# Kernel optimization log

Hardware: AMD Instinct MI355X
Metric: run time of the kernel (lower is better)

Reference implementation:

```python
import jax, jax.numpy as jnp
import numpy as np

B, L, N, C = 8, 33600, 128, 80
ALPHA, BETA, TOPK, EPS = 1.0, 6.0, 13, 1e-9


def setup_inputs() -> dict:
    key = jax.random.key(0)
    ks = jax.random.split(key, 7)
    pred_scores = jax.random.uniform(ks[0], (B, L, C), jnp.float32)  # post-sigmoid scores
    pc = jax.random.uniform(ks[1], (B, L, 2), jnp.float32) * 1024.0
    pwh = jax.random.uniform(ks[2], (B, L, 2), jnp.float32) * 128.0 + 8.0
    pred_boxes = jnp.concatenate([pc - pwh / 2, pc + pwh / 2], axis=-1)  # xyxy
    gc = jax.random.uniform(ks[3], (B, N, 2), jnp.float32) * 1024.0
    gwh = jax.random.uniform(ks[4], (B, N, 2), jnp.float32) * 256.0 + 16.0
    gt_boxes = jnp.concatenate([gc - gwh / 2, gc + gwh / 2], axis=-1)  # xyxy
    anchor_points = jax.random.uniform(ks[5], (1, L, 2), jnp.float32) * 1024.0
    gt_labels = jax.random.randint(ks[6], (B, N, 1), 0, C).astype(jnp.int64)
    # last quarter of GT slots are padding
    pad_gt_mask = (jnp.arange(N)[None, :, None] < 96).astype(jnp.float32)
    pad_gt_mask = jnp.broadcast_to(pad_gt_mask, (B, N, 1))
    return {"pred_scores": pred_scores, "pred_boxes": pred_boxes,
            "anchor_points": anchor_points, "gt_labels": gt_labels,
            "gt_boxes": gt_boxes, "pad_gt_mask": pad_gt_mask, "bg_index": C}


def _pairwise_iou(gt, pr):
    # gt: [B,N,4], pr: [B,L,4] xyxy -> iou [B,N,L]
    lt = jnp.maximum(gt[:, :, None, :2], pr[:, None, :, :2])
    rb = jnp.minimum(gt[:, :, None, 2:], pr[:, None, :, 2:])
    wh = jnp.clip(rb - lt, 0.0)
    inter = wh[..., 0] * wh[..., 1]
    area_g = ((gt[..., 2] - gt[..., 0]) * (gt[..., 3] - gt[..., 1]))[:, :, None]
    area_p = ((pr[..., 2] - pr[..., 0]) * (pr[..., 3] - pr[..., 1]))[:, None, :]
    iou = inter / (area_g + area_p - inter + EPS)
    iou = jnp.where(iou > 1.0 + EPS, 0.0, iou)
    return jnp.clip(jnp.nan_to_num(iou), 0.0, 1.0)


def reference(pred_scores, pred_boxes, anchor_points, gt_labels, gt_boxes, pad_gt_mask, bg_index):
    b, l, c = pred_scores.shape
    n = gt_boxes.shape[1]
    iou = _pairwise_iou(gt_boxes, pred_boxes)  # [B,N,L]

    # spatial containment of anchor points in horizontal gt boxes -> [B,N,L]
    pts = anchor_points[0]  # [L,2]
    spatial = ((pts[None, None, :, 0] >= gt_boxes[:, :, None, 0]) &
               (pts[None, None, :, 0] <= gt_boxes[:, :, None, 2]) &
               (pts[None, None, :, 1] >= gt_boxes[:, :, None, 1]) &
               (pts[None, None, :, 1] <= gt_boxes[:, :, None, 3]))

    # gather per-GT class scores: class_scores[b,n,l] = pred_scores[b,l,label[b,n]]
    lbl = jnp.clip(gt_labels[..., 0], 0, c - 1)  # [B,N]
    ps_t = jnp.transpose(pred_scores, (0, 2, 1))  # [B,C,L]
    class_scores = jnp.take_along_axis(ps_t, jnp.broadcast_to(lbl[:, :, None], (b, n, l)), axis=1)

    align = (class_scores ** ALPHA) * (iou ** BETA)  # [B,N,L]

    # top-k per GT over anchors
    k = min(TOPK, l)
    s = align * spatial.astype(align.dtype)
    _, topk_idx = jax.lax.top_k(s, k)  # [B,N,k]
    bidx = jnp.arange(b)[:, None, None]
    gidx = jnp.arange(n)[None, :, None]
    topk_mask = jnp.zeros((b, n, l), bool).at[bidx, gidx, topk_idx].set(True)
    topk_mask = topk_mask & (pad_gt_mask[..., 0] > 0)[:, :, None]

    positive = topk_mask.astype(align.dtype) * spatial.astype(align.dtype) * pad_gt_mask

    # conflict resolution: anchors matched to >1 GT keep only the best-IoU GT
    conflict = positive.sum(axis=1) > 1  # [B,L]
    best_gt = jnp.argmax(iou, axis=1)  # [B,L]
    best_mask = (jnp.arange(n)[None, :, None] == best_gt[:, None, :])  # [B,N,L]
    positive = jnp.where(conflict[:, None, :], positive * best_mask.astype(positive.dtype), positive)

    has_assign = positive.sum(axis=1) > 0  # [B,L]
    gt_idx = jnp.argmax(positive, axis=1)  # [B,L]
    assigned_labels = jnp.take_along_axis(gt_labels[..., 0], gt_idx, axis=1)  # [B,L]
    assigned_labels = jnp.where(has_assign, assigned_labels, bg_index)
    assigned_boxes = jnp.take_along_axis(gt_boxes, jnp.broadcast_to(gt_idx[:, :, None], (b, l, 4)), axis=1)

    masked_align = align * positive
    max_align = masked_align.max(axis=-1, keepdims=True)  # [B,N,1]
    max_iou = (iou * positive).max(axis=-1, keepdims=True)  # [B,N,1]
    norm_align = masked_align / (max_align + EPS) * max_iou
    norm_factor = norm_align.max(axis=1)  # [B,L]
    # scatter score at assigned class; bg labels (== C) one-hot to all-zero row
    assigned_scores = jax.nn.one_hot(assigned_labels, c, dtype=pred_scores.dtype)
    assigned_scores = assigned_scores * (norm_factor * has_assign.astype(norm_factor.dtype))[:, :, None]
    return assigned_labels, assigned_boxes, assigned_scores
```

## Files before the change

kernel.cpp:

```cpp
#include <hip/hip_runtime.h>
#include <cstdint>
#include <cstddef>

#define B_DIM 8
#define L_DIM 33600
#define N_DIM 128
#define C_DIM 80
#define K_TOP 13
#define EPS_F 1e-9f
#define CAP 4096

__device__ __forceinline__ float iou_pair(float g0, float g1, float g2, float g3,
                                          float p0, float p1, float p2, float p3) {
    float ltx = fmaxf(g0, p0), lty = fmaxf(g1, p1);
    float rbx = fminf(g2, p2), rby = fminf(g3, p3);
    float wx = fmaxf(__fsub_rn(rbx, ltx), 0.0f);
    float wy = fmaxf(__fsub_rn(rby, lty), 0.0f);
    float inter = __fmul_rn(wx, wy);
    float ag = __fmul_rn(__fsub_rn(g2, g0), __fsub_rn(g3, g1));
    float ap = __fmul_rn(__fsub_rn(p2, p0), __fsub_rn(p3, p1));
    float den = __fadd_rn(__fsub_rn(__fadd_rn(ag, ap), inter), EPS_F);
    float iou = __fdiv_rn(inter, den);
    if (iou > 1.0f) iou = 0.0f;
    iou = fminf(fmaxf(iou, 0.0f), 1.0f);
    return iou;
}

__device__ __forceinline__ unsigned long long make_key(double s, int l) {
    unsigned long long sb = (unsigned long long)__double_as_longlong(s);
    return (sb & 0xFFFFFFFFFFFF0000ull) | (unsigned long long)(0xFFFF - l);
}

__global__ __launch_bounds__(1024) void k_zero(
    int* __restrict__ cnt, float* __restrict__ maxal, float* __restrict__ maxio)
{
    const int t = threadIdx.x;
    cnt[t] = 0;
    maxal[t] = 0.0f;
    maxio[t] = 0.0f;
}

__global__ __launch_bounds__(256) void k_push(
    const float* __restrict__ pts, const float* __restrict__ gbox,
    const float* __restrict__ gpad,
    int* __restrict__ cnt, unsigned short* __restrict__ bucket,
    ulonglong2* __restrict__ spat, ulonglong2* __restrict__ posb2)
{
    const int b = blockIdx.y, t = threadIdx.x;
    __shared__ float4 gb[N_DIM];
    __shared__ float  gp[N_DIM];
    __shared__ int    lcnt[N_DIM];
    __shared__ int    gbase[N_DIM];
    if (t < N_DIM) {
        gb[t] = reinterpret_cast<const float4*>(gbox)[(size_t)b * N_DIM + t];
        gp[t] = gpad[b * N_DIM + t];
        lcnt[t] = 0;
    }
    __syncthreads();

    const int l = blockIdx.x * 256 + t;
    const bool inrange = (l < L_DIM);

    unsigned long long m0 = 0ull, m1 = 0ull;
    if (inrange) {
        posb2[(size_t)b * L_DIM + l] = make_ulonglong2(0ull, 0ull);
        const float2 ap = reinterpret_cast<const float2*>(pts)[l];
        for (int n = 0; n < N_DIM; ++n) {
            if (gp[n] <= 0.0f) continue;
            const float4 g = gb[n];
            bool in = (ap.x >= g.x && ap.x <= g.z && ap.y >= g.y && ap.y <= g.w);
            if (n < 64) m0 |= in ? (1ull << n) : 0ull;
            else        m1 |= in ? (1ull << (n - 64)) : 0ull;
        }
        spat[(size_t)b * L_DIM + l] = make_ulonglong2(m0, m1);
        if (l >= 32) {
            unsigned long long m = m0;
            while (m) { int n = __ffsll((long long)m) - 1; m &= m - 1; atomicAdd(&lcnt[n], 1); }
            m = m1;
            while (m) { int n = __ffsll((long long)m) - 1; m &= m - 1; atomicAdd(&lcnt[n + 64], 1); }
        }
    }
    __syncthreads();

    if (t < N_DIM) {
        int c = lcnt[t];
        gbase[t] = (c > 0) ? atomicAdd(&cnt[b * N_DIM + t], c) : 0;
        lcnt[t] = 0;
    }
    __syncthreads();

    if (inrange && l >= 32) {
        unsigned long long m = m0;
        while (m) {
            int n = __ffsll((long long)m) - 1; m &= m - 1;
            int pos = gbase[n] + atomicAdd(&lcnt[n], 1);
            if (pos < CAP) bucket[(size_t)(b * N_DIM + n) * CAP + pos] = (unsigned short)l;
        }
        m = m1;
        while (m) {
            int n = __ffsll((long long)m) - 1; m &= m - 1;
            int pos = gbase[n + 64] + atomicAdd(&lcnt[n + 64], 1);
            if (pos < CAP) bucket[(size_t)(b * N_DIM + n + 64) * CAP + pos] = (unsigned short)l;
        }
    }
}

__global__ __launch_bounds__(256) void k_top13(
    const float* __restrict__ psc, const float* __restrict__ pbox,
    const float* __restrict__ pts, const int* __restrict__ glbl,
    const float* __restrict__ gbox, const float* __restrict__ gpad,
    const int* __restrict__ cnt, const unsigned short* __restrict__ bucket,
    unsigned long long* __restrict__ posbits)
{
    const int n = blockIdx.x, b = blockIdx.y, t = threadIdx.x;
    if (gpad[b * N_DIM + n] <= 0.0f) return;

    const float g0 = gbox[(b * N_DIM + n) * 4 + 0];
    const float g1 = gbox[(b * N_DIM + n) * 4 + 1];
    const float g2 = gbox[(b * N_DIM + n) * 4 + 2];
    const float g3 = gbox[(b * N_DIM + n) * 4 + 3];
    int lbl = glbl[b * N_DIM + n];
    lbl = min(max(lbl, 0), C_DIM - 1);
    const float* psb = psc + (size_t)b * L_DIM * C_DIM;
    const float* pbb = pbox + (size_t)b * L_DIM * 4;
    const int bn = b * N_DIM + n;
    const int nc = min(cnt[bn], CAP);

    unsigned long long key[K_TOP];
    #pragma unroll
    for (int k = 0; k < K_TOP; ++k) key[k] = 0ull;

    for (int i = t; i < nc + 32; i += 256) {
        const int l = (i < 32) ? i : (int)bucket[(size_t)bn * CAP + (i - 32)];
        const float2 ap = reinterpret_cast<const float2*>(pts)[l];
        unsigned long long ck = (unsigned long long)(0xFFFF - l);
        if (ap.x >= g0 && ap.x <= g2 && ap.y >= g1 && ap.y <= g3) {
            const float4 pbv = reinterpret_cast<const float4*>(pbb)[l];
            float iou = iou_pair(g0, g1, g2, g3, pbv.x, pbv.y, pbv.z, pbv.w);
            if (iou > 0.0f) {
                float cs = psb[(size_t)l * C_DIM + lbl];
                double d = (double)iou, d2 = d * d;
                ck = make_key((double)cs * (d2 * d2 * d2), l);
            }
        }
        if (ck > key[K_TOP - 1]) {
            #pragma unroll
            for (int k = 0; k < K_TOP; ++k) {
                unsigned long long hi = key[k] > ck ? key[k] : ck;
                unsigned long long lo = key[k] > ck ? ck : key[k];
                key[k] = hi; ck = lo;
            }
        }
    }

    const int lane = t & 63, wid = t >> 6;
    __shared__ unsigned long long wl[4 * K_TOP];
    #pragma unroll 1
    for (int r = 0; r < K_TOP; ++r) {
        unsigned long long best = key[0];
        #pragma unroll
        for (int d = 1; d < 64; d <<= 1) {
            unsigned long long o = __shfl_xor(best, d, 64);
            best = o > best ? o : best;
        }
        if (key[0] == best && best != 0ull) {
            #pragma unroll
            for (int k = 0; k < K_TOP - 1; ++k) key[k] = key[k + 1];
            key[K_TOP - 1] = 0ull;
        }
        if (lane == 0) wl[wid * K_TOP + r] = best;
    }
    __syncthreads();
    if (wid != 0) return;

    unsigned long long v = (lane < 4 * K_TOP) ? wl[lane] : 0ull;
    #pragma unroll 1
    for (int r = 0; r < K_TOP; ++r) {
        unsigned long long best = v;
        #pragma unroll
        for (int d = 1; d < 64; d <<= 1) {
            unsigned long long o = __shfl_xor(best, d, 64);
            best = o > best ? o : best;
        }
        if (v == best) v = 0ull;
        if (lane == 0) {
            int win = 0xFFFF - (int)(best & 0xFFFFull);
            atomicOr(&posbits[((size_t)b * L_DIM + win) * 2 + (n >> 6)],
                     1ULL << (n & 63));
        }
    }
}

__global__ __launch_bounds__(256) void k_assign(
    const float* __restrict__ psc, const float* __restrict__ pbox,
    const int* __restrict__ glbl, const float* __restrict__ gbox,
    const unsigned long long* __restrict__ posbits,
    const ulonglong2* __restrict__ spat,
    const int* __restrict__ bgp,
    float* __restrict__ out_lab, float* __restrict__ out_box,
    int* __restrict__ fin_out, float* __restrict__ alat,
    float* __restrict__ maxal, float* __restrict__ maxio)
{
    const int b = blockIdx.y, t = threadIdx.x;
    const int l = blockIdx.x * 256 + t;
    __shared__ float4 gb[N_DIM];
    __shared__ int    gl[N_DIM];
    __shared__ int    qlist[256];
    __shared__ int    qn;
    if (t == 0) qn = 0;
    if (t < N_DIM) {
        gb[t] = reinterpret_cast<const float4*>(gbox)[(size_t)b * N_DIM + t];
        gl[t] = glbl[b * N_DIM + t];
    }
    __syncthreads();

    if (l < L_DIM) {
        const size_t bl = (size_t)b * L_DIM + l;
        const unsigned long long w0 = posbits[bl * 2 + 0];
        const unsigned long long w1 = posbits[bl * 2 + 1];
        const ulonglong2 sm = spat[bl];
        const unsigned long long p0 = w0 & sm.x, p1 = w1 & sm.y;
        const int pcnt = __popcll(p0) + __popcll(p1);

        if (pcnt <= 1) {
            int fin = (pcnt == 1) ? (p0 ? (__ffsll(p0) - 1) : (64 + __ffsll(p1) - 1)) : -1;
            out_lab[bl] = (fin >= 0) ? (float)gl[fin] : (float)bgp[0];
            int gidx = (fin >= 0) ? fin : 0;
            reinterpret_cast<float4*>(out_box)[bl] = gb[gidx];
            fin_out[bl] = fin;
            if (fin >= 0) {
                const float4 pb = reinterpret_cast<const float4*>(pbox)[bl];
                float4 g = gb[fin];
                float iou = iou_pair(g.x, g.y, g.z, g.w, pb.x, pb.y, pb.z, pb.w);
                int lb = min(max(gl[fin], 0), C_DIM - 1);
                float cs = psc[bl * C_DIM + lb];
                float al = cs * powf(iou, 6.0f);
                alat[bl] = al;
                atomicMax((int*)&maxal[b * N_DIM + fin], __float_as_int(al));
                atomicMax((int*)&maxio[b * N_DIM + fin], __float_as_int(iou));
            }
        } else {
            qlist[atomicAdd(&qn, 1)] = l;
        }
    }
    __syncthreads();

    const int lane = t & 63, wid = t >> 6;
    const int nq = qn;
    for (int i = wid; i < nq; i += 4) {
        const int ql = qlist[i];
        const size_t bl = (size_t)b * L_DIM + ql;
        const float4 pb = reinterpret_cast<const float4*>(pbox)[bl];
        float4 gA = gb[lane];
        float4 gB = gb[lane + 64];
        float iouA = iou_pair(gA.x, gA.y, gA.z, gA.w, pb.x, pb.y, pb.z, pb.w);
        float iouB = iou_pair(gB.x, gB.y, gB.z, gB.w, pb.x, pb.y, pb.z, pb.w);
        unsigned long long kA = ((unsigned long long)__float_as_uint(iouA) << 32)
                              | (unsigned long long)(0xFFFFFFFFu - (unsigned)lane);
        unsigned long long kB = ((unsigned long long)__float_as_uint(iouB) << 32)
                              | (unsigned long long)(0xFFFFFFFFu - (unsigned)(lane + 64));
        unsigned long long k = kA > kB ? kA : kB;
        #pragma unroll
        for (int d = 1; d < 64; d <<= 1) {
            unsigned long long o = __shfl_xor(k, d, 64);
            k = o > k ? o : k;
        }
        if (lane == 0) {
            int bestn = (int)(0xFFFFFFFFu - (unsigned)(k & 0xFFFFFFFFull));
            float bestiou = __uint_as_float((unsigned)(k >> 32));
            const unsigned long long w0 = posbits[bl * 2 + 0];
            const unsigned long long w1 = posbits[bl * 2 + 1];
            const ulonglong2 sm = spat[bl];
            const unsigned long long p0 = w0 & sm.x, p1 = w1 & sm.y;
            bool posbest = (bestn < 64) ? ((p0 >> bestn) & 1ull) : ((p1 >> (bestn - 64)) & 1ull);
            int fin = posbest ? bestn : -1;
            out_lab[bl] = (fin >= 0) ? (float)gl[fin] : (float)bgp[0];
            int gidx = (fin >= 0) ? fin : 0;
            reinterpret_cast<float4*>(out_box)[bl] = gb[gidx];
            fin_out[bl] = fin;
            if (fin >= 0) {
                int lb = min(max(gl[fin], 0), C_DIM - 1);
                float cs = psc[bl * C_DIM + lb];
                float al = cs * powf(bestiou, 6.0f);
                alat[bl] = al;
                atomicMax((int*)&maxal[b * N_DIM + fin], __float_as_int(al));
                atomicMax((int*)&maxio[b * N_DIM + fin], __float_as_int(bestiou));
            }
        }
    }
}

__global__ __launch_bounds__(256) void k_out(
    const int* __restrict__ fin_out, const float* __restrict__ alat,
    const float* __restrict__ maxal, const float* __restrict__ maxio,
    const int* __restrict__ glbl,
    float* __restrict__ outs)
{
    const int APB = 16;
    const int a0 = blockIdx.x * APB;
    const int t = threadIdx.x;
    __shared__ float snf[APB];
    __shared__ int   scl[APB];
    if (t < APB) {
        int a = a0 + t;
        float v = 0.0f; int c = -1;
        if (a < B_DIM * L_DIM) {
            int b = a / L_DIM;
            int fin = fin_out[a];
            if (fin >= 0) {
                v = alat[a] / (maxal[b * N_DIM + fin] + EPS_F) * maxio[b * N_DIM + fin];
                c = glbl[b * N_DIM + fin];
            }
        }
        snf[t] = v; scl[t] = c;
    }
    __syncthreads();
    float4* out4 = reinterpret_cast<float4*>(outs);
    for (int j = t; j < APB * 20; j += 256) {
        int ai = j / 20;
        int a = a0 + ai;
        if (a >= B_DIM * L_DIM) continue;
        int c0 = (j - ai * 20) * 4;
        float v = snf[ai]; int cl = scl[ai];
        float4 o;
        o.x = (c0 + 0 == cl) ? v : 0.0f;
        o.y = (c0 + 1 == cl) ? v : 0.0f;
        o.z = (c0 + 2 == cl) ? v : 0.0f;
        o.w = (c0 + 3 == cl) ? v : 0.0f;
        out4[(size_t)a * 20 + (j - ai * 20)] = o;
    }
}

extern "C" void kernel_launch(void* const* d_in, const int* in_sizes, int n_in,
                              void* d_out, int out_size, void* d_ws, size_t ws_size,
                              hipStream_t stream)
{
    const float* psc  = (const float*)d_in[0];
    const float* pbox = (const float*)d_in[1];
    const float* pts  = (const float*)d_in[2];
    const int*   glbl = (const int*)d_in[3];
    const float* gbox = (const float*)d_in[4];
    const float* gpad = (const float*)d_in[5];
    const int*   bgp  = (const int*)d_in[6];

    const size_t P = (size_t)B_DIM * L_DIM * 2 * sizeof(unsigned long long);
    char* w = (char*)d_ws;
    unsigned long long* posbits = (unsigned long long*)w;
    float* maxal = (float*)(w + P);
    float* maxio = (float*)(w + P + 4096);
    int*   cnt   = (int*)  (w + P + 8192);
    ulonglong2* spat = (ulonglong2*)(w + P + 12288);
    int*   fin   = (int*)  (w + 2 * P + 12288);
    float* alat  = (float*)(w + 2 * P + 12288 + 1075200);
    unsigned short* bucket = (unsigned short*)(w + 2 * P + 12288 + 2 * 1075200);

    float* out_lab = (float*)d_out;
    float* out_box = out_lab + (size_t)B_DIM * L_DIM;
    float* out_sc  = out_box + (size_t)B_DIM * L_DIM * 4;

    k_zero<<<dim3(1), dim3(1024), 0, stream>>>(cnt, maxal, maxio);
    k_push<<<dim3((L_DIM + 255) / 256, B_DIM), dim3(256), 0, stream>>>(
        pts, gbox, gpad, cnt, bucket, spat, (ulonglong2*)posbits);
    k_top13<<<dim3(N_DIM, B_DIM), dim3(256), 0, stream>>>(
        psc, pbox, pts, glbl, gbox, gpad, cnt, bucket, posbits);
    k_assign<<<dim3((L_DIM + 255) / 256, B_DIM), dim3(256), 0, stream>>>(
        psc, pbox, glbl, gbox, posbits, spat, bgp,
        out_lab, out_box, fin, alat, maxal, maxio);
    k_out<<<dim3((B_DIM * L_DIM + 15) / 16), dim3(256), 0, stream>>>(
        fin, alat, maxal, maxio, glbl, out_sc);
}
```

Baseline: 90.44 us.

## Replace global atomic bucket counters with per-chunk segments and prefix-sum lookup

Removes the zeroing kernel and the global atomicAdd-based bucket allocation, writing each chunk's candidate anchors into fixed-size per-chunk segments with per-chunk counts. The top-13 kernel builds a prefix sum over chunk counts and binary-searches it to find each candidate. This saves a launch and a second pass in k_push, but adds a serial scan and a binary search per candidate, and silently truncates when a chunk holds more than 96 anchors inside one GT.

```diff
diff --git a/kernel.cpp b/kernel.cpp
--- a/kernel.cpp
+++ b/kernel.cpp
@@ -8,7 +8,8 @@
 #define C_DIM 80
 #define K_TOP 13
 #define EPS_F 1e-9f
-#define CAP 4096
+#define NCHUNK 132
+#define SEGSZ 96
 
 __device__ __forceinline__ float iou_pair(float g0, float g1, float g2, float g3,
                                           float p0, float p1, float p2, float p3) {
@@ -31,40 +32,32 @@
     return (sb & 0xFFFFFFFFFFFF0000ull) | (unsigned long long)(0xFFFF - l);
 }
 
-__global__ __launch_bounds__(1024) void k_zero(
-    int* __restrict__ cnt, float* __restrict__ maxal, float* __restrict__ maxio)
-{
-    const int t = threadIdx.x;
-    cnt[t] = 0;
-    maxal[t] = 0.0f;
-    maxio[t] = 0.0f;
-}
-
 __global__ __launch_bounds__(256) void k_push(
     const float* __restrict__ pts, const float* __restrict__ gbox,
     const float* __restrict__ gpad,
-    int* __restrict__ cnt, unsigned short* __restrict__ bucket,
-    ulonglong2* __restrict__ spat, ulonglong2* __restrict__ posb2)
-{
-    const int b = blockIdx.y, t = threadIdx.x;
+    int* __restrict__ scount, unsigned short* __restrict__ bucket,
+    ulonglong2* __restrict__ spat, ulonglong2* __restrict__ posb2,
+    float* __restrict__ maxal, float* __restrict__ maxio)
+{
+    const int chunk = blockIdx.x, b = blockIdx.y, t = threadIdx.x;
     __shared__ float4 gb[N_DIM];
     __shared__ float  gp[N_DIM];
     __shared__ int    lcnt[N_DIM];
-    __shared__ int    gbase[N_DIM];
     if (t < N_DIM) {
         gb[t] = reinterpret_cast<const float4*>(gbox)[(size_t)b * N_DIM + t];
         gp[t] = gpad[b * N_DIM + t];
         lcnt[t] = 0;
-    }
-    __syncthreads();
-
-    const int l = blockIdx.x * 256 + t;
+        if (chunk == 0) { maxal[b * N_DIM + t] = 0.0f; maxio[b * N_DIM + t] = 0.0f; }
+    }
+    __syncthreads();
+
+    const int l = chunk * 256 + t;
     const bool inrange = (l < L_DIM);
 
-    unsigned long long m0 = 0ull, m1 = 0ull;
     if (inrange) {
         posb2[(size_t)b * L_DIM + l] = make_ulonglong2(0ull, 0ull);
         const float2 ap = reinterpret_cast<const float2*>(pts)[l];
+        unsigned long long m0 = 0ull, m1 = 0ull;
         for (int n = 0; n < N_DIM; ++n) {
             if (gp[n] <= 0.0f) continue;
             const float4 g = gb[n];
@@ -74,42 +67,32 @@
         }
         spat[(size_t)b * L_DIM + l] = make_ulonglong2(m0, m1);
         if (l >= 32) {
+            const size_t segbase = ((size_t)(b * N_DIM) * NCHUNK + chunk) * SEGSZ;
             unsigned long long m = m0;
-            while (m) { int n = __ffsll((long long)m) - 1; m &= m - 1; atomicAdd(&lcnt[n], 1); }
+            while (m) {
+                int n = __ffsll((long long)m) - 1; m &= m - 1;
+                int pos = atomicAdd(&lcnt[n], 1);
+                if (pos < SEGSZ) bucket[segbase + (size_t)n * NCHUNK * SEGSZ + pos] = (unsigned short)l;
+            }
             m = m1;
-            while (m) { int n = __ffsll((long long)m) - 1; m &= m - 1; atomicAdd(&lcnt[n + 64], 1); }
-        }
-    }
-    __syncthreads();
-
-    if (t < N_DIM) {
-        int c = lcnt[t];
-        gbase[t] = (c > 0) ? atomicAdd(&cnt[b * N_DIM + t], c) : 0;
-        lcnt[t] = 0;
-    }
-    __syncthreads();
-
-    if (inrange && l >= 32) {
-        unsigned long long m = m0;
-        while (m) {
-            int n = __ffsll((long long)m) - 1; m &= m - 1;
-            int pos = gbase[n] + atomicAdd(&lcnt[n], 1);
-            if (pos < CAP) bucket[(size_t)(b * N_DIM + n) * CAP + pos] = (unsigned short)l;
-        }
-        m = m1;
-        while (m) {
-            int n = __ffsll((long long)m) - 1; m &= m - 1;
-            int pos = gbase[n + 64] + atomicAdd(&lcnt[n + 64], 1);
-            if (pos < CAP) bucket[(size_t)(b * N_DIM + n + 64) * CAP + pos] = (unsigned short)l;
-        }
-    }
+            while (m) {
+                int n = __ffsll((long long)m) - 1; m &= m - 1;
+                int pos = atomicAdd(&lcnt[n + 64], 1);
+                if (pos < SEGSZ) bucket[segbase + (size_t)(n + 64) * NCHUNK * SEGSZ + pos] = (unsigned short)l;
+            }
+        }
+    }
+    __syncthreads();
+
+    if (t < N_DIM)
+        scount[(b * N_DIM + t) * NCHUNK + chunk] = min(lcnt[t], SEGSZ);
 }
 
 __global__ __launch_bounds__(256) void k_top13(
     const float* __restrict__ psc, const float* __restrict__ pbox,
     const float* __restrict__ pts, const int* __restrict__ glbl,
     const float* __restrict__ gbox, const float* __restrict__ gpad,
-    const int* __restrict__ cnt, const unsigned short* __restrict__ bucket,
+    const int* __restrict__ scount, const unsigned short* __restrict__ bucket,
     unsigned long long* __restrict__ posbits)
 {
     const int n = blockIdx.x, b = blockIdx.y, t = threadIdx.x;
@@ -124,14 +107,28 @@
     const float* psb = psc + (size_t)b * L_DIM * C_DIM;
     const float* pbb = pbox + (size_t)b * L_DIM * 4;
     const int bn = b * N_DIM + n;
-    const int nc = min(cnt[bn], CAP);
+
+    __shared__ int pfx[NCHUNK + 1];
+    if (t < NCHUNK) pfx[t + 1] = scount[bn * NCHUNK + t];
+    __syncthreads();
+    if (t == 0) { pfx[0] = 0; for (int i = 1; i <= NCHUNK; ++i) pfx[i] += pfx[i - 1]; }
+    __syncthreads();
+    const int nc = pfx[NCHUNK];
+    const unsigned short* seg = bucket + (size_t)bn * NCHUNK * SEGSZ;
 
     unsigned long long key[K_TOP];
     #pragma unroll
     for (int k = 0; k < K_TOP; ++k) key[k] = 0ull;
 
     for (int i = t; i < nc + 32; i += 256) {
-        const int l = (i < 32) ? i : (int)bucket[(size_t)bn * CAP + (i - 32)];
+        int l;
+        if (i < 32) l = i;
+        else {
+            const int ci = i - 32;
+            int lo = 0, hi = NCHUNK - 1;
+            while (lo < hi) { int mid = (lo + hi + 1) >> 1; if (pfx[mid] <= ci) lo = mid; else hi = mid - 1; }
+            l = (int)seg[(size_t)lo * SEGSZ + (ci - pfx[lo])];
+        }
         const float2 ap = reinterpret_cast<const float2*>(pts)[l];
         unsigned long long ck = (unsigned long long)(0xFFFF - l);
         if (ap.x >= g0 && ap.x <= g2 && ap.y >= g1 && ap.y <= g3) {
@@ -348,21 +345,20 @@
     unsigned long long* posbits = (unsigned long long*)w;
     float* maxal = (float*)(w + P);
     float* maxio = (float*)(w + P + 4096);
-    int*   cnt   = (int*)  (w + P + 8192);
-    ulonglong2* spat = (ulonglong2*)(w + P + 12288);
-    int*   fin   = (int*)  (w + 2 * P + 12288);
-    float* alat  = (float*)(w + 2 * P + 12288 + 1075200);
-    unsigned short* bucket = (unsigned short*)(w + 2 * P + 12288 + 2 * 1075200);
+    int*   scount = (int*) (w + P + 8192);
+    ulonglong2* spat = (ulonglong2*)(w + P + 8192 + 540672);
+    int*   fin   = (int*)  (w + 2 * P + 8192 + 540672);
+    float* alat  = (float*)(w + 2 * P + 8192 + 540672 + 1075200);
+    unsigned short* bucket = (unsigned short*)(w + 2 * P + 8192 + 540672 + 2 * 1075200);
 
     float* out_lab = (float*)d_out;
     float* out_box = out_lab + (size_t)B_DIM * L_DIM;
     float* out_sc  = out_box + (size_t)B_DIM * L_DIM * 4;
 
-    k_zero<<<dim3(1), dim3(1024), 0, stream>>>(cnt, maxal, maxio);
-    k_push<<<dim3((L_DIM + 255) / 256, B_DIM), dim3(256), 0, stream>>>(
-        pts, gbox, gpad, cnt, bucket, spat, (ulonglong2*)posbits);
+    k_push<<<dim3(NCHUNK, B_DIM), dim3(256), 0, stream>>>(
+        pts, gbox, gpad, scount, bucket, spat, (ulonglong2*)posbits, maxal, maxio);
     k_top13<<<dim3(N_DIM, B_DIM), dim3(256), 0, stream>>>(
-        psc, pbox, pts, glbl, gbox, gpad, cnt, bucket, posbits);
+        psc, pbox, pts, glbl, gbox, gpad, scount, bucket, posbits);
     k_assign<<<dim3((L_DIM + 255) / 256, B_DIM), dim3(256), 0, stream>>>(
         psc, pbox, glbl, gbox, posbits, spat, bgp,
         out_lab, out_box, fin, alat, maxal, maxio);
```

After: 91.16 us. No clear change (+0.8%).
